# Performance work log

Hardware: AMD Instinct MI355X
Metric: run time of the kernel (lower is better)

Reference implementation:

```python
import jax, jax.numpy as jnp
import numpy as np


def _conv1x1(x, w, b):
    # x: (B,C,H,W), w: (O,C), b: (O,)
    return jnp.einsum('oc,bchw->bohw', w, x) + b[None, :, None, None]


def _avg_pool2(x):
    B, C, H, W = x.shape
    return x.reshape(B, C, H // 2, 2, W // 2, 2).mean(axis=(3, 5))


def setup_inputs() -> dict:
    key = jax.random.key(0)
    B, C, H, W = 8, 64, 64, 64
    ks = jax.random.split(key, 14)
    s = 1.0 / np.sqrt(C)

    def wb(k1, k2):
        return (jax.random.uniform(k1, (C, C), jnp.float32, -s, s),
                jax.random.uniform(k2, (C,), jnp.float32, -s, s))

    w_q, b_q = wb(ks[0], ks[1])
    w_K, b_K = wb(ks[2], ks[3])
    w_V, b_V = wb(ks[4], ks[5])
    w_Q, b_Q = wb(ks[6], ks[7])
    w_k, b_k = wb(ks[8], ks[9])
    w_v, b_v = wb(ks[10], ks[11])
    x = jax.random.normal(ks[12], (B, C, H, W), jnp.float32)
    gamma = jnp.ones((1,), jnp.float32)
    return dict(x=x, w_q=w_q, b_q=b_q, w_K=w_K, b_K=b_K, w_V=w_V, b_V=b_V,
                w_Q=w_Q, b_Q=b_Q, w_k=w_k, b_k=b_k, w_v=w_v, b_v=b_v,
                gamma=gamma)


def reference(x, w_q, b_q, w_K, b_K, w_V, b_V, w_Q, b_Q, w_k, b_k, w_v, b_v, gamma):
    B, C, H, W = x.shape
    N = H * W
    N4 = N // 4

    # Stage 1: pooled queries vs full key/value
    q = _conv1x1(x, w_q, b_q)                      # (B,C,H,W); torch views as (B,C,W,H) but H==W
    qp = _avg_pool2(q).reshape(B, C, N4).transpose(0, 2, 1)   # (B,N/4,C)
    Kf = _conv1x1(x, w_K, b_K).reshape(B, C, N)                # (B,C,N)
    Vf = _conv1x1(x, w_V, b_V).reshape(B, C, N)                # (B,C,N)
    attn = jax.nn.softmax(jnp.einsum('bnc,bcm->bnm', qp, Kf), axis=-1)  # (B,N/4,N)
    out = jnp.einsum('bcm,bnm->bcn', Vf, attn)                 # (B,C,N/4)
    out = out.reshape(B, C, H // 2, W // 2)

    # Stage 2: full queries vs pooled-derived key/value
    Qf = _conv1x1(x, w_Q, b_Q).reshape(B, C, N).transpose(0, 2, 1)  # (B,N,C)
    kp = _conv1x1(out, w_k, b_k).reshape(B, C, N4)                  # (B,C,N/4)
    vp = _conv1x1(out, w_v, b_v).reshape(B, C, N4)                  # (B,C,N/4)
    attn2 = jax.nn.softmax(jnp.einsum('bnc,bcm->bnm', Qf, kp), axis=-1)  # (B,N,N/4)
    out2 = jnp.einsum('bcm,bnm->bcn', vp, attn2).reshape(B, C, H, W)

    return gamma * out2 + x
```

## Files before the change

kernel.cpp:

```cpp
#include <hip/hip_runtime.h>
#include <math.h>


typedef __bf16 bf16;
typedef __attribute__((ext_vector_type(4))) __bf16 bf16x4;
typedef __attribute__((ext_vector_type(8))) __bf16 bf16x8;
typedef __attribute__((ext_vector_type(4))) float f32x4;

__device__ __forceinline__ void gl_lds16(const bf16* g, bf16* l) {
    __builtin_amdgcn_global_load_lds(
        (const __attribute__((address_space(1))) unsigned int*)g,
        (__attribute__((address_space(3))) unsigned int*)l,
        16, 0, 0);
}

__device__ __forceinline__ void proj_wave(
    const bf16* __restrict__ src, int TN,
    const float* __restrict__ W, const float* __restrict__ Bs,
    bf16* __restrict__ Y, int tr, int N, int b, int gn0, int lane)
{
    const int c16 = lane & 15, q4 = lane >> 4;
    bf16x8 wa[4][2];
    #pragma unroll
    for (int to = 0; to < 4; ++to)
        #pragma unroll
        for (int h = 0; h < 2; ++h) {
            const float* wp = W + (16 * to + c16) * 64 + q4 * 8 + 32 * h;
            float4 f0 = *(const float4*)wp;
            float4 f1 = *(const float4*)(wp + 4);
            bf16 tmp[8] = {(bf16)f0.x, (bf16)f0.y, (bf16)f0.z, (bf16)f0.w,
                           (bf16)f1.x, (bf16)f1.y, (bf16)f1.z, (bf16)f1.w};
            wa[to][h] = *(bf16x8*)tmp;
        }
    for (int tn = 0; tn < TN; ++tn) {
        bf16x8 xb0 = *(const bf16x8*)&src[(16 * tn + c16) * 72 + q4 * 8];
        bf16x8 xb1 = *(const bf16x8*)&src[(16 * tn + c16) * 72 + q4 * 8 + 32];
        #pragma unroll
        for (int to = 0; to < 4; ++to) {
            f32x4 acc = (f32x4){0.f, 0.f, 0.f, 0.f};
            acc = __builtin_amdgcn_mfma_f32_16x16x32_bf16(wa[to][0], xb0, acc, 0, 0, 0);
            acc = __builtin_amdgcn_mfma_f32_16x16x32_bf16(wa[to][1], xb1, acc, 0, 0, 0);
            if (tr) {
                float4 b4 = *(const float4*)(Bs + 16 * to + q4 * 4);
                bf16x4 yv;
                yv[0] = (bf16)(acc[0] + b4.x); yv[1] = (bf16)(acc[1] + b4.y);
                yv[2] = (bf16)(acc[2] + b4.z); yv[3] = (bf16)(acc[3] + b4.w);
                *(bf16x4*)(Y + ((size_t)b * N + gn0 + 16 * tn + c16) * 64 + 16 * to + q4 * 4) = yv;
            } else {
                float4 b4 = *(const float4*)(Bs + 16 * to + q4 * 4);
                float bias[4] = {b4.x, b4.y, b4.z, b4.w};
                #pragma unroll
                for (int r = 0; r < 4; ++r)
                    Y[((size_t)b * 64 + 16 * to + q4 * 4 + r) * N + gn0 + 16 * tn + c16] =
                        (bf16)(acc[r] + bias[r]);
            }
        }
    }
}

__global__ __launch_bounds__(256) void prep_kernel(
    const float* __restrict__ x,
    const float* __restrict__ w_K, const float* __restrict__ b_K, bf16* __restrict__ Kt,
    const float* __restrict__ w_Q, const float* __restrict__ b_Q, bf16* __restrict__ Qt,
    const float* __restrict__ w_V, const float* __restrict__ b_V, bf16* __restrict__ Vf,
    const float* __restrict__ w_q, const float* __restrict__ b_q, bf16* __restrict__ qpt)
{
    __shared__ float tile[128 * 65];
    __shared__ __align__(16) bf16 xbT[128 * 72];
    __shared__ __align__(16) bf16 xpb[32 * 72];
    const int t  = threadIdx.x;
    const int h2 = blockIdx.x;
    const int b  = blockIdx.y;
    const int n0 = h2 * 128;

    #pragma unroll
    for (int i = 0; i < 32; ++i) {
        int lin = i * 256 + t;
        int n = lin & 127, c = lin >> 7;
        tile[n * 65 + c] = x[((size_t)b * 64 + c) * 4096 + n0 + n];
    }
    __syncthreads();
    #pragma unroll
    for (int i = 0; i < 4; ++i) {
        int slot = i * 256 + t;
        int n = slot >> 3, c0 = (slot & 7) * 8;
        bf16 tmp[8];
        #pragma unroll
        for (int j = 0; j < 8; ++j) tmp[j] = (bf16)tile[n * 65 + c0 + j];
        *(bf16x8*)&xbT[n * 72 + c0] = *(bf16x8*)tmp;
    }
    {
        int wp = t & 31, c0 = (t >> 5) * 8;
        bf16 tmp[8];
        #pragma unroll
        for (int j = 0; j < 8; ++j) {
            float a = tile[(2 * wp) * 65 + c0 + j] + tile[(2 * wp + 1) * 65 + c0 + j]
                    + tile[(64 + 2 * wp) * 65 + c0 + j] + tile[(64 + 2 * wp + 1) * 65 + c0 + j];
            tmp[j] = (bf16)(0.25f * a);
        }
        *(bf16x8*)&xpb[wp * 72 + c0] = *(bf16x8*)tmp;
    }
    __syncthreads();

    const int lane = t & 63;
    const int w    = t >> 6;
    {
        const int mat  = w >> 1;
        const int half = w & 1;
        proj_wave(xbT + half * 64 * 72, 4,
                  mat == 0 ? w_K : w_Q, mat == 0 ? b_K : b_Q,
                  mat == 0 ? Kt : Qt, 1, 4096, b, n0 + half * 64, lane);
    }
    if (w < 2) {
        proj_wave(xbT + w * 64 * 72, 4, w_V, b_V, Vf, 0, 4096, b, n0 + w * 64, lane);
    } else if (w == 2) {
        proj_wave(xpb, 2, w_q, b_q, qpt, 1, 1024, b, h2 * 32, lane);
    }
}

template<int NSPLIT, int MODE, int U>
__global__ __launch_bounds__(256, 3) void flash_kernel(
    const bf16* __restrict__ Qt, const bf16* __restrict__ Kt,
    const bf16* __restrict__ Vn, int NQ, int L,
    bf16* __restrict__ Opart, float* __restrict__ Lbuf,
    float* __restrict__ out_f, const float* __restrict__ resid,
    const float* __restrict__ gamma_p)
{
    const int tid  = threadIdx.x;
    const int lane = tid & 63;
    const int w    = tid >> 6;
    const int c16  = lane & 15;
    const int q4   = lane >> 4;
    const int b    = blockIdx.y;
    const int n0   = blockIdx.x * (64 * U) + w * (16 * U);
    const int s    = (NSPLIT > 1) ? blockIdx.z : 0;
    const int SL   = L / NSPLIT;
    const int k0   = s * SL;
    const int ntiles = SL / 64;

    __shared__ __align__(16) bf16 Ks[2][64 * 64];
    __shared__ __align__(16) bf16 Vs[2][64 * 64];
    __shared__ __align__(16) bf16 Pw[4][16 * U * 72];

    const int rl8 = lane >> 3;
    const int cg  = ((lane & 7) - rl8) & 7;

    const bf16* Kb = Kt + (size_t)b * L * 64;
    const bf16* Vb = Vn + (size_t)b * 64 * L;

    bf16x8 bq[U][2];
    #pragma unroll
    for (int u = 0; u < U; ++u) {
        const bf16* qrow = Qt + ((size_t)b * NQ + n0 + 16 * u + c16) * 64 + q4 * 8;
        bq[u][0] = *(const bf16x8*)(qrow);
        bq[u][1] = *(const bf16x8*)(qrow + 32);
    }

    f32x4 O[U][4];
    #pragma unroll
    for (int u = 0; u < U; ++u)
        #pragma unroll
        for (int g = 0; g < 4; ++g) O[u][g] = (f32x4){0.f, 0.f, 0.f, 0.f};
    float l_acc[U];
    #pragma unroll
    for (int u = 0; u < U; ++u) l_acc[u] = 0.f;

    #pragma unroll
    for (int j = 0; j < 2; ++j) {
        const int row = 16 * w + 8 * j + rl8;
        gl_lds16(Kb + (size_t)(k0 + row) * 64 + cg * 8, &Ks[0][(16 * w + 8 * j) * 64]);
        gl_lds16(Vb + (size_t)row * L + k0 + cg * 8,    &Vs[0][(16 * w + 8 * j) * 64]);
    }
    __syncthreads();

    for (int it = 0; it < ntiles; ++it) {
        const int buf = it & 1;
        if (it + 1 < ntiles) {
            const int kn = k0 + (it + 1) * 64;
            #pragma unroll
            for (int j = 0; j < 2; ++j) {
                const int row = 16 * w + 8 * j + rl8;
                gl_lds16(Kb + (size_t)(kn + row) * 64 + cg * 8, &Ks[buf ^ 1][(16 * w + 8 * j) * 64]);
                gl_lds16(Vb + (size_t)row * L + kn + cg * 8,    &Vs[buf ^ 1][(16 * w + 8 * j) * 64]);
            }
        }

        f32x4 sv[U][4];
        #pragma unroll
        for (int t = 0; t < 4; ++t) {
            const bf16* krow = &Ks[buf][(16 * t + c16) * 64];
            bf16x8 ak0 = *(const bf16x8*)&krow[((q4 + c16) & 7) * 8];
            bf16x8 ak1 = *(const bf16x8*)&krow[((q4 + 4 + c16) & 7) * 8];
            #pragma unroll
            for (int u = 0; u < U; ++u) {
                f32x4 z = (f32x4){0.f, 0.f, 0.f, 0.f};
                z = __builtin_amdgcn_mfma_f32_16x16x32_bf16(ak0, bq[u][0], z, 0, 0, 0);
                sv[u][t] = __builtin_amdgcn_mfma_f32_16x16x32_bf16(ak1, bq[u][1], z, 0, 0, 0);
            }
        }

        #pragma unroll
        for (int u = 0; u < U; ++u) {
            #pragma unroll
            for (int t = 0; t < 4; ++t) {
                #pragma unroll
                for (int r = 0; r < 4; ++r) {
                    float p = __expf(sv[u][t][r]);
                    sv[u][t][r] = p;
                    l_acc[u] += p;
                }
                bf16x4 pv;
                pv[0] = (bf16)sv[u][t][0]; pv[1] = (bf16)sv[u][t][1];
                pv[2] = (bf16)sv[u][t][2]; pv[3] = (bf16)sv[u][t][3];
                *(bf16x4*)&Pw[w][(16 * u + c16) * 72 + 16 * t + 4 * q4] = pv;
            }
        }

        #pragma unroll
        for (int h = 0; h < 2; ++h) {
            bf16x8 pf[U];
            #pragma unroll
            for (int u = 0; u < U; ++u)
                pf[u] = *(const bf16x8*)&Pw[w][(16 * u + c16) * 72 + 32 * h + 8 * q4];
            #pragma unroll
            for (int g = 0; g < 4; ++g) {
                bf16x8 av = *(const bf16x8*)&Vs[buf][(16 * g + c16) * 64 + ((4 * h + q4 + c16) & 7) * 8];
                #pragma unroll
                for (int u = 0; u < U; ++u)
                    O[u][g] = __builtin_amdgcn_mfma_f32_16x16x32_bf16(av, pf[u], O[u][g], 0, 0, 0);
            }
        }
        __syncthreads();
    }

    float l_tot[U];
    #pragma unroll
    for (int u = 0; u < U; ++u) {
        float l = l_acc[u];
        l += __shfl_xor(l, 16);
        l += __shfl_xor(l, 32);
        l_tot[u] = l;
    }

    if (MODE == 2) {
        const float gm = gamma_p[0];
        #pragma unroll
        for (int u = 0; u < U; ++u) {
            float inv = gm / l_tot[u];
            const int n = n0 + 16 * u + c16;
            #pragma unroll
            for (int g = 0; g < 4; ++g) {
                #pragma unroll
                for (int r = 0; r < 4; ++r) {
                    size_t oidx = ((size_t)b * 64 + 16 * g + 4 * q4 + r) * NQ + n;
                    out_f[oidx] = O[u][g][r] * inv + resid[oidx];
                }
            }
        }
    } else {
        #pragma unroll
        for (int u = 0; u < U; ++u) {
            float inv = 1.0f / l_tot[u];
            bf16* dst = Opart + ((size_t)(b * NSPLIT + s) * NQ + n0 + 16 * u + c16) * 64 + q4 * 4;
            #pragma unroll
            for (int g = 0; g < 4; ++g) {
                bf16x4 yv;
                #pragma unroll
                for (int r = 0; r < 4; ++r) yv[r] = (bf16)(O[u][g][r] * inv);
                *(bf16x4*)(dst + 16 * g) = yv;
            }
        }
        if (lane < 16) {
            #pragma unroll
            for (int u = 0; u < U; ++u)
                Lbuf[(b * NSPLIT + s) * NQ + n0 + 16 * u + lane] = l_tot[u];
        }
    }
}

__global__ __launch_bounds__(256) void comb1kv_kernel(
    const bf16* __restrict__ Opart, const float* __restrict__ Lbuf,
    const float* __restrict__ w_k, const float* __restrict__ b_k, bf16* __restrict__ kpt,
    const float* __restrict__ w_v, const float* __restrict__ b_v, bf16* __restrict__ vp)
{
    __shared__ __align__(16) bf16 tile[32 * 72];
    __shared__ float wbuf[32 * 8];
    const int t  = threadIdx.x;
    const int m0 = blockIdx.x * 32;
    const int b  = blockIdx.y;

    if (t < 32) {
        int m = m0 + t;
        float ls[8], lt = 0.f;
        #pragma unroll
        for (int s = 0; s < 8; ++s) {
            ls[s] = Lbuf[(b * 8 + s) * 1024 + m];
            lt += ls[s];
        }
        float inv = 1.f / lt;
        #pragma unroll
        for (int s = 0; s < 8; ++s) wbuf[t * 8 + s] = ls[s] * inv;
    }
    __syncthreads();

    #pragma unroll
    for (int i = 0; i < 2; ++i) {
        int ml = i * 16 + (t >> 4);
        int c4 = (t & 15) * 4;
        const bf16* base = Opart + ((size_t)(b * 8) * 1024 + m0 + ml) * 64 + c4;
        float a0 = 0.f, a1 = 0.f, a2 = 0.f, a3 = 0.f;
        #pragma unroll
        for (int s = 0; s < 8; ++s) {
            bf16x4 v = *(const bf16x4*)(base + (size_t)s * 1024 * 64);
            float wg = wbuf[ml * 8 + s];
            a0 += (float)v[0] * wg; a1 += (float)v[1] * wg;
            a2 += (float)v[2] * wg; a3 += (float)v[3] * wg;
        }
        bf16x4 o; o[0] = (bf16)a0; o[1] = (bf16)a1; o[2] = (bf16)a2; o[3] = (bf16)a3;
        *(bf16x4*)&tile[ml * 72 + c4] = o;
    }
    __syncthreads();

    const int lane = t & 63;
    const int w    = t >> 6;
    const int c16 = lane & 15, q4 = lane >> 4;

    if (w < 2) {
        bf16x8 wb[4][2];
        #pragma unroll
        for (int to = 0; to < 4; ++to)
            #pragma unroll
            for (int h = 0; h < 2; ++h) {
                const float* wp = w_k + (16 * to + c16) * 64 + q4 * 8 + 32 * h;
                float4 f0 = *(const float4*)wp;
                float4 f1 = *(const float4*)(wp + 4);
                bf16 tmp[8] = {(bf16)f0.x, (bf16)f0.y, (bf16)f0.z, (bf16)f0.w,
                               (bf16)f1.x, (bf16)f1.y, (bf16)f1.z, (bf16)f1.w};
                wb[to][h] = *(bf16x8*)tmp;
            }
        const int tm = w;
        bf16x8 a0 = *(const bf16x8*)&tile[(16 * tm + c16) * 72 + q4 * 8];
        bf16x8 a1 = *(const bf16x8*)&tile[(16 * tm + c16) * 72 + q4 * 8 + 32];
        #pragma unroll
        for (int to = 0; to < 4; ++to) {
            f32x4 acc = (f32x4){0.f, 0.f, 0.f, 0.f};
            acc = __builtin_amdgcn_mfma_f32_16x16x32_bf16(a0, wb[to][0], acc, 0, 0, 0);
            acc = __builtin_amdgcn_mfma_f32_16x16x32_bf16(a1, wb[to][1], acc, 0, 0, 0);
            float bias = b_k[16 * to + c16];
            #pragma unroll
            for (int r = 0; r < 4; ++r)
                kpt[((size_t)b * 1024 + m0 + 16 * tm + 4 * q4 + r) * 64 + 16 * to + c16] =
                    (bf16)(acc[r] + bias);
        }
    } else {
        bf16x8 wa[4][2];
        #pragma unroll
        for (int ta = 0; ta < 4; ++ta)
            #pragma unroll
            for (int h = 0; h < 2; ++h) {
                const float* wp = w_v + (16 * ta + c16) * 64 + q4 * 8 + 32 * h;
                float4 f0 = *(const float4*)wp;
                float4 f1 = *(const float4*)(wp + 4);
                bf16 tmp[8] = {(bf16)f0.x, (bf16)f0.y, (bf16)f0.z, (bf16)f0.w,
                               (bf16)f1.x, (bf16)f1.y, (bf16)f1.z, (bf16)f1.w};
                wa[ta][h] = *(bf16x8*)tmp;
            }
        const int tm = w - 2;
        bf16x8 bb0 = *(const bf16x8*)&tile[(16 * tm + c16) * 72 + q4 * 8];
        bf16x8 bb1 = *(const bf16x8*)&tile[(16 * tm + c16) * 72 + q4 * 8 + 32];
        #pragma unroll
        for (int ta = 0; ta < 4; ++ta) {
            f32x4 acc = (f32x4){0.f, 0.f, 0.f, 0.f};
            acc = __builtin_amdgcn_mfma_f32_16x16x32_bf16(wa[ta][0], bb0, acc, 0, 0, 0);
            acc = __builtin_amdgcn_mfma_f32_16x16x32_bf16(wa[ta][1], bb1, acc, 0, 0, 0);
            float4 b4 = *(const float4*)(b_v + 16 * ta + 4 * q4);
            float bias[4] = {b4.x, b4.y, b4.z, b4.w};
            #pragma unroll
            for (int r = 0; r < 4; ++r)
                vp[((size_t)b * 64 + 16 * ta + 4 * q4 + r) * 1024 + m0 + 16 * tm + c16] =
                    (bf16)(acc[r] + bias[r]);
        }
    }
}

extern "C" void kernel_launch(void* const* d_in, const int* in_sizes, int n_in,
                              void* d_out, int out_size, void* d_ws, size_t ws_size,
                              hipStream_t stream) {
    const float* x    = (const float*)d_in[0];
    const float* w_q  = (const float*)d_in[1];
    const float* b_q  = (const float*)d_in[2];
    const float* w_K  = (const float*)d_in[3];
    const float* b_K  = (const float*)d_in[4];
    const float* w_V  = (const float*)d_in[5];
    const float* b_V  = (const float*)d_in[6];
    const float* w_Q  = (const float*)d_in[7];
    const float* b_Q  = (const float*)d_in[8];
    const float* w_k  = (const float*)d_in[9];
    const float* b_k  = (const float*)d_in[10];
    const float* w_v  = (const float*)d_in[11];
    const float* b_v  = (const float*)d_in[12];
    const float* gamma = (const float*)d_in[13];
    float* out = (float*)d_out;

    char* ws = (char*)d_ws;
    bf16*  Kt    = (bf16*)ws;   ws += (size_t)8 * 4096 * 64 * 2;
    bf16*  Qt    = (bf16*)ws;   ws += (size_t)8 * 4096 * 64 * 2;
    bf16*  Vf    = (bf16*)ws;   ws += (size_t)8 * 4096 * 64 * 2;
    bf16*  qpt   = (bf16*)ws;   ws += (size_t)8 * 1024 * 64 * 2;
    bf16*  kpt   = (bf16*)ws;   ws += (size_t)8 * 1024 * 64 * 2;
    bf16*  vp    = (bf16*)ws;   ws += (size_t)8 * 64 * 1024 * 2;
    bf16*  Opart = (bf16*)ws;   ws += (size_t)8 * 8 * 1024 * 64 * 2;
    float* Lb    = (float*)ws;  ws += (size_t)8 * 8 * 1024 * 4;

    prep_kernel<<<dim3(32, 8), 256, 0, stream>>>(
        x, w_K, b_K, Kt, w_Q, b_Q, Qt, w_V, b_V, Vf, w_q, b_q, qpt);

    flash_kernel<8, 1, 1><<<dim3(16, 8, 8), 256, 0, stream>>>(
        qpt, Kt, Vf, 1024, 4096, Opart, Lb, nullptr, nullptr, nullptr);

    comb1kv_kernel<<<dim3(32, 8), 256, 0, stream>>>(
        Opart, Lb, w_k, b_k, kpt, w_v, b_v, vp);

    flash_kernel<1, 2, 1><<<dim3(64, 8, 1), 256, 0, stream>>>(
        Qt, kpt, vp, 4096, 1024, nullptr, nullptr, out, x, gamma);
}
```

Measured before the change: 137.3 us.

## Split stage-2 attention over keys and add fp32 combine kernel

Stage-2 flash attention now splits the 1024 keys into two partitions. Each partition writes normalized fp32 partial outputs and row sums to workspace, and a new combine kernel merges them, transposes through LDS, applies gamma and adds the residual. Stage 1 also changes its template tile parameter and halves its grid's x dimension. The split is meant to raise parallelism for the under-occupied stage-2 launch, at the cost of an extra kernel launch and an extra fp32 round trip of the output through global memory.

```diff
diff --git a/kernel.cpp b/kernel.cpp
--- a/kernel.cpp
+++ b/kernel.cpp
@@ -261,13 +261,24 @@
         #pragma unroll
         for (int u = 0; u < U; ++u) {
             float inv = 1.0f / l_tot[u];
-            bf16* dst = Opart + ((size_t)(b * NSPLIT + s) * NQ + n0 + 16 * u + c16) * 64 + q4 * 4;
-            #pragma unroll
-            for (int g = 0; g < 4; ++g) {
-                bf16x4 yv;
-                #pragma unroll
-                for (int r = 0; r < 4; ++r) yv[r] = (bf16)(O[u][g][r] * inv);
-                *(bf16x4*)(dst + 16 * g) = yv;
+            if (MODE == 1) {
+                bf16* dst = Opart + ((size_t)(b * NSPLIT + s) * NQ + n0 + 16 * u + c16) * 64 + q4 * 4;
+                #pragma unroll
+                for (int g = 0; g < 4; ++g) {
+                    bf16x4 yv;
+                    #pragma unroll
+                    for (int r = 0; r < 4; ++r) yv[r] = (bf16)(O[u][g][r] * inv);
+                    *(bf16x4*)(dst + 16 * g) = yv;
+                }
+            } else {
+                float* dst = out_f + ((size_t)(b * NSPLIT + s) * NQ + n0 + 16 * u + c16) * 64 + q4 * 4;
+                #pragma unroll
+                for (int g = 0; g < 4; ++g) {
+                    float4 yv;
+                    yv.x = O[u][g][0] * inv; yv.y = O[u][g][1] * inv;
+                    yv.z = O[u][g][2] * inv; yv.w = O[u][g][3] * inv;
+                    *(float4*)(dst + 16 * g) = yv;
+                }
             }
         }
         if (lane < 16) {
@@ -380,6 +391,49 @@
                 vp[((size_t)b * 64 + 16 * ta + 4 * q4 + r) * 1024 + m0 + 16 * tm + c16] =
                     (bf16)(acc[r] + bias[r]);
         }
+    }
+}
+
+__global__ __launch_bounds__(256) void comb2_kernel(
+    const float* __restrict__ Of2, const float* __restrict__ Lb2,
+    const float* __restrict__ x, const float* __restrict__ gamma_p,
+    float* __restrict__ out)
+{
+    __shared__ float tile[64][65];
+    __shared__ float wt[64][2];
+    const int t  = threadIdx.x;
+    const int q0 = blockIdx.x * 64;
+    const int b  = blockIdx.y;
+
+    if (t < 64) {
+        float l0 = Lb2[((size_t)b * 2 + 0) * 4096 + q0 + t];
+        float l1 = Lb2[((size_t)b * 2 + 1) * 4096 + q0 + t];
+        float inv = 1.f / (l0 + l1);
+        wt[t][0] = l0 * inv; wt[t][1] = l1 * inv;
+    }
+    __syncthreads();
+
+    #pragma unroll
+    for (int i = 0; i < 4; ++i) {
+        int lin = i * 256 + t;
+        int q = lin >> 4, c4 = (lin & 15) * 4;
+        float w0 = wt[q][0], w1 = wt[q][1];
+        float4 v0 = *(const float4*)&Of2[(((size_t)b * 2 + 0) * 4096 + q0 + q) * 64 + c4];
+        float4 v1 = *(const float4*)&Of2[(((size_t)b * 2 + 1) * 4096 + q0 + q) * 64 + c4];
+        tile[q][c4 + 0] = w0 * v0.x + w1 * v1.x;
+        tile[q][c4 + 1] = w0 * v0.y + w1 * v1.y;
+        tile[q][c4 + 2] = w0 * v0.z + w1 * v1.z;
+        tile[q][c4 + 3] = w0 * v0.w + w1 * v1.w;
+    }
+    __syncthreads();
+
+    const float gm = gamma_p[0];
+    const int wv = t >> 6, ln = t & 63;
+    #pragma unroll
+    for (int cc = 0; cc < 16; ++cc) {
+        int c = wv * 16 + cc;
+        size_t o = ((size_t)b * 64 + c) * 4096 + q0 + ln;
+        out[o] = gm * tile[ln][c] + x[o];
     }
 }
 
@@ -411,16 +465,21 @@
     bf16*  vp    = (bf16*)ws;   ws += (size_t)8 * 64 * 1024 * 2;
     bf16*  Opart = (bf16*)ws;   ws += (size_t)8 * 8 * 1024 * 64 * 2;
     float* Lb    = (float*)ws;  ws += (size_t)8 * 8 * 1024 * 4;
+    float* Of2   = (float*)ws;  ws += (size_t)8 * 2 * 4096 * 64 * 4;
+    float* Lb2   = (float*)ws;  ws += (size_t)8 * 2 * 4096 * 4;
 
     prep_kernel<<<dim3(32, 8), 256, 0, stream>>>(
         x, w_K, b_K, Kt, w_Q, b_Q, Qt, w_V, b_V, Vf, w_q, b_q, qpt);
 
-    flash_kernel<8, 1, 1><<<dim3(16, 8, 8), 256, 0, stream>>>(
+    flash_kernel<8, 1, 2><<<dim3(8, 8, 8), 256, 0, stream>>>(
         qpt, Kt, Vf, 1024, 4096, Opart, Lb, nullptr, nullptr, nullptr);
 
     comb1kv_kernel<<<dim3(32, 8), 256, 0, stream>>>(
         Opart, Lb, w_k, b_k, kpt, w_v, b_v, vp);
 
-    flash_kernel<1, 2, 1><<<dim3(64, 8, 1), 256, 0, stream>>>(
-        Qt, kpt, vp, 4096, 1024, nullptr, nullptr, out, x, gamma);
-}
+    flash_kernel<2, 3, 2><<<dim3(32, 8, 2), 256, 0, stream>>>(
+        Qt, kpt, vp, 4096, 1024, nullptr, Lb2, Of2, nullptr, nullptr);
+
+    comb2_kernel<<<dim3(64, 8), 256, 0, stream>>>(
+        Of2, Lb2, x, gamma, out);
+}
```

New measurement: 142.8 us. 1.04x slower.

## Fold K/V/Q projections into pooled side via algebraic reassociation

Applied to the files above, without the earlier changes.

Stops materialising the full-resolution K, V and Q projections. Stage 1 now attends raw bf16 x against the query premultiplied by W_K^T, and applies W_V after the softmax-weighted sum of x. The K-bias term cancels in softmax, and the Q-bias enters stage 2 as a per-key additive bias. The flash kernel also gains U=2 query unrolling and, for stage 2, a 512-thread two-way key split with an LDS reduction. This removes three large projection GEMMs and their bf16 writes, in exchange for extra small projections in the combine kernel and a bias load in the inner loop.

```diff
diff --git a/kernel.cpp b/kernel.cpp
--- a/kernel.cpp
+++ b/kernel.cpp
@@ -14,45 +14,69 @@
         16, 0, 0);
 }
 
-__device__ __forceinline__ void proj_wave(
-    const bf16* __restrict__ src, int TN,
-    const float* __restrict__ W, const float* __restrict__ Bs,
-    bf16* __restrict__ Y, int tr, int N, int b, int gn0, int lane)
+struct WFrag { bf16x8 f[4][2]; };
+
+template<int WT>
+__device__ __forceinline__ WFrag load_wfrag(const float* __restrict__ W, int lane) {
+    const int c16 = lane & 15, q4 = lane >> 4;
+    WFrag wf;
+    #pragma unroll
+    for (int to = 0; to < 4; ++to)
+        #pragma unroll
+        for (int h = 0; h < 2; ++h) {
+            bf16 tmp[8];
+            if (WT == 0) {
+                const float* wp = W + (16 * to + c16) * 64 + q4 * 8 + 32 * h;
+                float4 f0 = *(const float4*)wp;
+                float4 f1 = *(const float4*)(wp + 4);
+                tmp[0] = (bf16)f0.x; tmp[1] = (bf16)f0.y;
+                tmp[2] = (bf16)f0.z; tmp[3] = (bf16)f0.w;
+                tmp[4] = (bf16)f1.x; tmp[5] = (bf16)f1.y;
+                tmp[6] = (bf16)f1.z; tmp[7] = (bf16)f1.w;
+            } else {
+                #pragma unroll
+                for (int j = 0; j < 8; ++j)
+                    tmp[j] = (bf16)W[(q4 * 8 + 32 * h + j) * 64 + 16 * to + c16];
+            }
+            wf.f[to][h] = *(bf16x8*)tmp;
+        }
+    return wf;
+}
+
+template<int OUT>
+__device__ __forceinline__ void proj_run(
+    const bf16* __restrict__ src, int TN, const WFrag& wf, const float* __restrict__ Bs,
+    bf16* __restrict__ Y, int N, int b, int gn0, bf16* __restrict__ Yl, int lane)
 {
     const int c16 = lane & 15, q4 = lane >> 4;
-    bf16x8 wa[4][2];
-    #pragma unroll
-    for (int to = 0; to < 4; ++to)
-        #pragma unroll
-        for (int h = 0; h < 2; ++h) {
-            const float* wp = W + (16 * to + c16) * 64 + q4 * 8 + 32 * h;
-            float4 f0 = *(const float4*)wp;
-            float4 f1 = *(const float4*)(wp + 4);
-            bf16 tmp[8] = {(bf16)f0.x, (bf16)f0.y, (bf16)f0.z, (bf16)f0.w,
-                           (bf16)f1.x, (bf16)f1.y, (bf16)f1.z, (bf16)f1.w};
-            wa[to][h] = *(bf16x8*)tmp;
-        }
     for (int tn = 0; tn < TN; ++tn) {
         bf16x8 xb0 = *(const bf16x8*)&src[(16 * tn + c16) * 72 + q4 * 8];
         bf16x8 xb1 = *(const bf16x8*)&src[(16 * tn + c16) * 72 + q4 * 8 + 32];
         #pragma unroll
         for (int to = 0; to < 4; ++to) {
             f32x4 acc = (f32x4){0.f, 0.f, 0.f, 0.f};
-            acc = __builtin_amdgcn_mfma_f32_16x16x32_bf16(wa[to][0], xb0, acc, 0, 0, 0);
-            acc = __builtin_amdgcn_mfma_f32_16x16x32_bf16(wa[to][1], xb1, acc, 0, 0, 0);
-            if (tr) {
+            acc = __builtin_amdgcn_mfma_f32_16x16x32_bf16(wf.f[to][0], xb0, acc, 0, 0, 0);
+            acc = __builtin_amdgcn_mfma_f32_16x16x32_bf16(wf.f[to][1], xb1, acc, 0, 0, 0);
+            float bias[4] = {0.f, 0.f, 0.f, 0.f};
+            if (Bs) {
                 float4 b4 = *(const float4*)(Bs + 16 * to + q4 * 4);
+                bias[0] = b4.x; bias[1] = b4.y; bias[2] = b4.z; bias[3] = b4.w;
+            }
+            if (OUT == 0) {
                 bf16x4 yv;
-                yv[0] = (bf16)(acc[0] + b4.x); yv[1] = (bf16)(acc[1] + b4.y);
-                yv[2] = (bf16)(acc[2] + b4.z); yv[3] = (bf16)(acc[3] + b4.w);
-                *(bf16x4*)(Y + ((size_t)b * N + gn0 + 16 * tn + c16) * 64 + 16 * to + q4 * 4) = yv;
+                #pragma unroll
+                for (int r = 0; r < 4; ++r) yv[r] = (bf16)(acc[r] + bias[r]);
+                *(bf16x4*)(Y + ((size_t)b * N + gn0 + 16 * tn + c16) * 64 + 16 * to + 4 * q4) = yv;
+            } else if (OUT == 1) {
+                #pragma unroll
+                for (int r = 0; r < 4; ++r)
+                    Y[((size_t)b * 64 + 16 * to + 4 * q4 + r) * N + gn0 + 16 * tn + c16] =
+                        (bf16)(acc[r] + bias[r]);
             } else {
-                float4 b4 = *(const float4*)(Bs + 16 * to + q4 * 4);
-                float bias[4] = {b4.x, b4.y, b4.z, b4.w};
-                #pragma unroll
-                for (int r = 0; r < 4; ++r)
-                    Y[((size_t)b * 64 + 16 * to + q4 * 4 + r) * N + gn0 + 16 * tn + c16] =
-                        (bf16)(acc[r] + bias[r]);
+                bf16x4 yv;
+                #pragma unroll
+                for (int r = 0; r < 4; ++r) yv[r] = (bf16)(acc[r] + bias[r]);
+                *(bf16x4*)&Yl[(16 * tn + c16) * 72 + 16 * to + 4 * q4] = yv;
             }
         }
     }
@@ -60,14 +84,13 @@
 
 __global__ __launch_bounds__(256) void prep_kernel(
     const float* __restrict__ x,
-    const float* __restrict__ w_K, const float* __restrict__ b_K, bf16* __restrict__ Kt,
-    const float* __restrict__ w_Q, const float* __restrict__ b_Q, bf16* __restrict__ Qt,
-    const float* __restrict__ w_V, const float* __restrict__ b_V, bf16* __restrict__ Vf,
-    const float* __restrict__ w_q, const float* __restrict__ b_q, bf16* __restrict__ qpt)
+    const float* __restrict__ w_q, const float* __restrict__ b_q,
+    const float* __restrict__ w_K,
+    bf16* __restrict__ xt, bf16* __restrict__ xn, bf16* __restrict__ qkt)
 {
     __shared__ float tile[128 * 65];
-    __shared__ __align__(16) bf16 xbT[128 * 72];
     __shared__ __align__(16) bf16 xpb[32 * 72];
+    __shared__ __align__(16) bf16 qtile[32 * 72];
     const int t  = threadIdx.x;
     const int h2 = blockIdx.x;
     const int b  = blockIdx.y;
@@ -80,6 +103,19 @@
         tile[n * 65 + c] = x[((size_t)b * 64 + c) * 4096 + n0 + n];
     }
     __syncthreads();
+    {
+        int wp = t & 31, c0 = (t >> 5) * 8;
+        bf16 tmp[8];
+        #pragma unroll
+        for (int j = 0; j < 8; ++j) {
+            float a = tile[(2 * wp) * 65 + c0 + j] + tile[(2 * wp + 1) * 65 + c0 + j]
+                    + tile[(64 + 2 * wp) * 65 + c0 + j] + tile[(64 + 2 * wp + 1) * 65 + c0 + j];
+            tmp[j] = (bf16)(0.25f * a);
+        }
+        *(bf16x8*)&xpb[wp * 72 + c0] = *(bf16x8*)tmp;
+    }
+    __syncthreads();
+
     #pragma unroll
     for (int i = 0; i < 4; ++i) {
         int slot = i * 256 + t;
@@ -87,60 +123,52 @@
         bf16 tmp[8];
         #pragma unroll
         for (int j = 0; j < 8; ++j) tmp[j] = (bf16)tile[n * 65 + c0 + j];
-        *(bf16x8*)&xbT[n * 72 + c0] = *(bf16x8*)tmp;
-    }
-    {
-        int wp = t & 31, c0 = (t >> 5) * 8;
+        *(bf16x8*)&xt[((size_t)b * 4096 + n0 + n) * 64 + c0] = *(bf16x8*)tmp;
+    }
+    #pragma unroll
+    for (int i = 0; i < 4; ++i) {
+        int slot = i * 256 + t;
+        int c = slot >> 4, n8 = slot & 15;
         bf16 tmp[8];
         #pragma unroll
-        for (int j = 0; j < 8; ++j) {
-            float a = tile[(2 * wp) * 65 + c0 + j] + tile[(2 * wp + 1) * 65 + c0 + j]
-                    + tile[(64 + 2 * wp) * 65 + c0 + j] + tile[(64 + 2 * wp + 1) * 65 + c0 + j];
-            tmp[j] = (bf16)(0.25f * a);
-        }
-        *(bf16x8*)&xpb[wp * 72 + c0] = *(bf16x8*)tmp;
-    }
-    __syncthreads();
-
-    const int lane = t & 63;
-    const int w    = t >> 6;
-    {
-        const int mat  = w >> 1;
-        const int half = w & 1;
-        proj_wave(xbT + half * 64 * 72, 4,
-                  mat == 0 ? w_K : w_Q, mat == 0 ? b_K : b_Q,
-                  mat == 0 ? Kt : Qt, 1, 4096, b, n0 + half * 64, lane);
-    }
-    if (w < 2) {
-        proj_wave(xbT + w * 64 * 72, 4, w_V, b_V, Vf, 0, 4096, b, n0 + w * 64, lane);
-    } else if (w == 2) {
-        proj_wave(xpb, 2, w_q, b_q, qpt, 1, 1024, b, h2 * 32, lane);
-    }
-}
-
-template<int NSPLIT, int MODE, int U>
-__global__ __launch_bounds__(256, 3) void flash_kernel(
+        for (int j = 0; j < 8; ++j) tmp[j] = (bf16)tile[(n8 * 8 + j) * 65 + c];
+        *(bf16x8*)&xn[((size_t)b * 64 + c) * 4096 + n0 + n8 * 8] = *(bf16x8*)tmp;
+    }
+    if ((t >> 6) == 3) {
+        const int lane = t & 63;
+        WFrag wfq  = load_wfrag<0>(w_q, lane);
+        WFrag wfKT = load_wfrag<1>(w_K, lane);
+        proj_run<2>(xpb, 2, wfq, b_q, nullptr, 0, 0, 0, qtile, lane);
+        asm volatile("s_waitcnt lgkmcnt(0)" ::: "memory");
+        proj_run<0>(qtile, 2, wfKT, nullptr, qkt, 1024, b, h2 * 32, nullptr, lane);
+    }
+}
+
+template<int NSPLIT, int MODE, int U, int KS, bool BIAS>
+__global__ __launch_bounds__(256 * KS, KS == 1 ? 3 : 2) void flash_kernel(
     const bf16* __restrict__ Qt, const bf16* __restrict__ Kt,
     const bf16* __restrict__ Vn, int NQ, int L,
     bf16* __restrict__ Opart, float* __restrict__ Lbuf,
     float* __restrict__ out_f, const float* __restrict__ resid,
-    const float* __restrict__ gamma_p)
+    const float* __restrict__ gamma_p, const float* __restrict__ Gb)
 {
     const int tid  = threadIdx.x;
     const int lane = tid & 63;
     const int w    = tid >> 6;
+    const int wl   = w & 3;
+    const int g    = w >> 2;
     const int c16  = lane & 15;
     const int q4   = lane >> 4;
     const int b    = blockIdx.y;
-    const int n0   = blockIdx.x * (64 * U) + w * (16 * U);
+    const int n0   = blockIdx.x * (64 * U) + wl * (16 * U);
     const int s    = (NSPLIT > 1) ? blockIdx.z : 0;
-    const int SL   = L / NSPLIT;
-    const int k0   = s * SL;
+    const int SL   = L / (NSPLIT * KS);
+    const int k0   = (s * KS + g) * SL;
     const int ntiles = SL / 64;
 
-    __shared__ __align__(16) bf16 Ks[2][64 * 64];
-    __shared__ __align__(16) bf16 Vs[2][64 * 64];
-    __shared__ __align__(16) bf16 Pw[4][16 * U * 72];
+    __shared__ __align__(16) bf16 Ks[KS][2][64 * 64];
+    __shared__ __align__(16) bf16 Vs[KS][2][64 * 64];
+    __shared__ __align__(16) bf16 Pw[4 * KS][16 * U * 72];
 
     const int rl8 = lane >> 3;
     const int cg  = ((lane & 7) - rl8) & 7;
@@ -160,16 +188,16 @@
     #pragma unroll
     for (int u = 0; u < U; ++u)
         #pragma unroll
-        for (int g = 0; g < 4; ++g) O[u][g] = (f32x4){0.f, 0.f, 0.f, 0.f};
+        for (int gi = 0; gi < 4; ++gi) O[u][gi] = (f32x4){0.f, 0.f, 0.f, 0.f};
     float l_acc[U];
     #pragma unroll
     for (int u = 0; u < U; ++u) l_acc[u] = 0.f;
 
     #pragma unroll
     for (int j = 0; j < 2; ++j) {
-        const int row = 16 * w + 8 * j + rl8;
-        gl_lds16(Kb + (size_t)(k0 + row) * 64 + cg * 8, &Ks[0][(16 * w + 8 * j) * 64]);
-        gl_lds16(Vb + (size_t)row * L + k0 + cg * 8,    &Vs[0][(16 * w + 8 * j) * 64]);
+        const int row = 16 * wl + 8 * j + rl8;
+        gl_lds16(Kb + (size_t)(k0 + row) * 64 + cg * 8, &Ks[g][0][(16 * wl + 8 * j) * 64]);
+        gl_lds16(Vb + (size_t)row * L + k0 + cg * 8,    &Vs[g][0][(16 * wl + 8 * j) * 64]);
     }
     __syncthreads();
 
@@ -179,16 +207,16 @@
             const int kn = k0 + (it + 1) * 64;
             #pragma unroll
             for (int j = 0; j < 2; ++j) {
-                const int row = 16 * w + 8 * j + rl8;
-                gl_lds16(Kb + (size_t)(kn + row) * 64 + cg * 8, &Ks[buf ^ 1][(16 * w + 8 * j) * 64]);
-                gl_lds16(Vb + (size_t)row * L + kn + cg * 8,    &Vs[buf ^ 1][(16 * w + 8 * j) * 64]);
+                const int row = 16 * wl + 8 * j + rl8;
+                gl_lds16(Kb + (size_t)(kn + row) * 64 + cg * 8, &Ks[g][buf ^ 1][(16 * wl + 8 * j) * 64]);
+                gl_lds16(Vb + (size_t)row * L + kn + cg * 8,    &Vs[g][buf ^ 1][(16 * wl + 8 * j) * 64]);
             }
         }
 
         f32x4 sv[U][4];
         #pragma unroll
         for (int t = 0; t < 4; ++t) {
-            const bf16* krow = &Ks[buf][(16 * t + c16) * 64];
+            const bf16* krow = &Ks[g][buf][(16 * t + c16) * 64];
             bf16x8 ak0 = *(const bf16x8*)&krow[((q4 + c16) & 7) * 8];
             bf16x8 ak1 = *(const bf16x8*)&krow[((q4 + 4 + c16) & 7) * 8];
             #pragma unroll
@@ -199,13 +227,22 @@
             }
         }
 
+        float4 gb[4];
+        if (BIAS) {
+            #pragma unroll
+            for (int t = 0; t < 4; ++t)
+                gb[t] = *(const float4*)&Gb[(size_t)b * 1024 + k0 + it * 64 + 16 * t + 4 * q4];
+        }
+
         #pragma unroll
         for (int u = 0; u < U; ++u) {
             #pragma unroll
             for (int t = 0; t < 4; ++t) {
                 #pragma unroll
                 for (int r = 0; r < 4; ++r) {
-                    float p = __expf(sv[u][t][r]);
+                    float sval = sv[u][t][r];
+                    if (BIAS) sval += ((const float*)&gb[t])[r];
+                    float p = __expf(sval);
                     sv[u][t][r] = p;
                     l_acc[u] += p;
                 }
@@ -223,11 +260,11 @@
             for (int u = 0; u < U; ++u)
                 pf[u] = *(const bf16x8*)&Pw[w][(16 * u + c16) * 72 + 32 * h + 8 * q4];
             #pragma unroll
-            for (int g = 0; g < 4; ++g) {
-                bf16x8 av = *(const bf16x8*)&Vs[buf][(16 * g + c16) * 64 + ((4 * h + q4 + c16) & 7) * 8];
+            for (int gi = 0; gi < 4; ++gi) {
+                bf16x8 av = *(const bf16x8*)&Vs[g][buf][(16 * gi + c16) * 64 + ((4 * h + q4 + c16) & 7) * 8];
                 #pragma unroll
                 for (int u = 0; u < U; ++u)
-                    O[u][g] = __builtin_amdgcn_mfma_f32_16x16x32_bf16(av, pf[u], O[u][g], 0, 0, 0);
+                    O[u][gi] = __builtin_amdgcn_mfma_f32_16x16x32_bf16(av, pf[u], O[u][gi], 0, 0, 0);
             }
         }
         __syncthreads();
@@ -242,6 +279,33 @@
         l_tot[u] = l;
     }
 
+    if (KS == 2) {
+        float* sc = (float*)&Pw[0][0];
+        const int base = (wl * 64 + lane) * 34;
+        if (g == 1) {
+            #pragma unroll
+            for (int u = 0; u < U; ++u) {
+                #pragma unroll
+                for (int gi = 0; gi < 4; ++gi)
+                    #pragma unroll
+                    for (int r = 0; r < 4; ++r)
+                        sc[base + u * 16 + gi * 4 + r] = O[u][gi][r];
+                sc[base + 32 + u] = l_tot[u];
+            }
+        }
+        __syncthreads();
+        if (g == 1) return;
+        #pragma unroll
+        for (int u = 0; u < U; ++u) {
+            #pragma unroll
+            for (int gi = 0; gi < 4; ++gi)
+                #pragma unroll
+                for (int r = 0; r < 4; ++r)
+                    O[u][gi][r] += sc[base + u * 16 + gi * 4 + r];
+            l_tot[u] += sc[base + 32 + u];
+        }
+    }
+
     if (MODE == 2) {
         const float gm = gamma_p[0];
         #pragma unroll
@@ -249,11 +313,11 @@
             float inv = gm / l_tot[u];
             const int n = n0 + 16 * u + c16;
             #pragma unroll
-            for (int g = 0; g < 4; ++g) {
+            for (int gi = 0; gi < 4; ++gi) {
                 #pragma unroll
                 for (int r = 0; r < 4; ++r) {
-                    size_t oidx = ((size_t)b * 64 + 16 * g + 4 * q4 + r) * NQ + n;
-                    out_f[oidx] = O[u][g][r] * inv + resid[oidx];
+                    size_t oidx = ((size_t)b * 64 + 16 * gi + 4 * q4 + r) * NQ + n;
+                    out_f[oidx] = O[u][gi][r] * inv + resid[oidx];
                 }
             }
         }
@@ -263,11 +327,11 @@
             float inv = 1.0f / l_tot[u];
             bf16* dst = Opart + ((size_t)(b * NSPLIT + s) * NQ + n0 + 16 * u + c16) * 64 + q4 * 4;
             #pragma unroll
-            for (int g = 0; g < 4; ++g) {
+            for (int gi = 0; gi < 4; ++gi) {
                 bf16x4 yv;
                 #pragma unroll
-                for (int r = 0; r < 4; ++r) yv[r] = (bf16)(O[u][g][r] * inv);
-                *(bf16x4*)(dst + 16 * g) = yv;
+                for (int r = 0; r < 4; ++r) yv[r] = (bf16)(O[u][gi][r] * inv);
+                *(bf16x4*)(dst + 16 * gi) = yv;
             }
         }
         if (lane < 16) {
@@ -280,14 +344,27 @@
 
 __global__ __launch_bounds__(256) void comb1kv_kernel(
     const bf16* __restrict__ Opart, const float* __restrict__ Lbuf,
-    const float* __restrict__ w_k, const float* __restrict__ b_k, bf16* __restrict__ kpt,
-    const float* __restrict__ w_v, const float* __restrict__ b_v, bf16* __restrict__ vp)
+    const float* __restrict__ w_V, const float* __restrict__ b_V,
+    const float* __restrict__ w_k, const float* __restrict__ b_k,
+    const float* __restrict__ w_v, const float* __restrict__ b_v,
+    const float* __restrict__ w_Q, const float* __restrict__ b_Q,
+    bf16* __restrict__ qk2t, bf16* __restrict__ vp, float* __restrict__ Gb)
 {
     __shared__ __align__(16) bf16 tile[32 * 72];
+    __shared__ __align__(16) bf16 otile[32 * 72];
+    __shared__ __align__(16) bf16 kpl[32 * 72];
     __shared__ float wbuf[32 * 8];
     const int t  = threadIdx.x;
     const int m0 = blockIdx.x * 32;
     const int b  = blockIdx.y;
+    const int w  = t >> 6;
+    const int lane = t & 63;
+
+    WFrag wf;
+    if      (w == 0) wf = load_wfrag<0>(w_V, lane);
+    else if (w == 1) wf = load_wfrag<0>(w_k, lane);
+    else if (w == 2) wf = load_wfrag<0>(w_v, lane);
+    else             wf = load_wfrag<1>(w_Q, lane);
 
     if (t < 32) {
         int m = m0 + t;
@@ -321,65 +398,17 @@
     }
     __syncthreads();
 
-    const int lane = t & 63;
-    const int w    = t >> 6;
-    const int c16 = lane & 15, q4 = lane >> 4;
-
-    if (w < 2) {
-        bf16x8 wb[4][2];
-        #pragma unroll
-        for (int to = 0; to < 4; ++to)
-            #pragma unroll
-            for (int h = 0; h < 2; ++h) {
-                const float* wp = w_k + (16 * to + c16) * 64 + q4 * 8 + 32 * h;
-                float4 f0 = *(const float4*)wp;
-                float4 f1 = *(const float4*)(wp + 4);
-                bf16 tmp[8] = {(bf16)f0.x, (bf16)f0.y, (bf16)f0.z, (bf16)f0.w,
-                               (bf16)f1.x, (bf16)f1.y, (bf16)f1.z, (bf16)f1.w};
-                wb[to][h] = *(bf16x8*)tmp;
-            }
-        const int tm = w;
-        bf16x8 a0 = *(const bf16x8*)&tile[(16 * tm + c16) * 72 + q4 * 8];
-        bf16x8 a1 = *(const bf16x8*)&tile[(16 * tm + c16) * 72 + q4 * 8 + 32];
-        #pragma unroll
-        for (int to = 0; to < 4; ++to) {
-            f32x4 acc = (f32x4){0.f, 0.f, 0.f, 0.f};
-            acc = __builtin_amdgcn_mfma_f32_16x16x32_bf16(a0, wb[to][0], acc, 0, 0, 0);
-            acc = __builtin_amdgcn_mfma_f32_16x16x32_bf16(a1, wb[to][1], acc, 0, 0, 0);
-            float bias = b_k[16 * to + c16];
-            #pragma unroll
-            for (int r = 0; r < 4; ++r)
-                kpt[((size_t)b * 1024 + m0 + 16 * tm + 4 * q4 + r) * 64 + 16 * to + c16] =
-                    (bf16)(acc[r] + bias);
-        }
-    } else {
-        bf16x8 wa[4][2];
-        #pragma unroll
-        for (int ta = 0; ta < 4; ++ta)
-            #pragma unroll
-            for (int h = 0; h < 2; ++h) {
-                const float* wp = w_v + (16 * ta + c16) * 64 + q4 * 8 + 32 * h;
-                float4 f0 = *(const float4*)wp;
-                float4 f1 = *(const float4*)(wp + 4);
-                bf16 tmp[8] = {(bf16)f0.x, (bf16)f0.y, (bf16)f0.z, (bf16)f0.w,
-                               (bf16)f1.x, (bf16)f1.y, (bf16)f1.z, (bf16)f1.w};
-                wa[ta][h] = *(bf16x8*)tmp;
-            }
-        const int tm = w - 2;
-        bf16x8 bb0 = *(const bf16x8*)&tile[(16 * tm + c16) * 72 + q4 * 8];
-        bf16x8 bb1 = *(const bf16x8*)&tile[(16 * tm + c16) * 72 + q4 * 8 + 32];
-        #pragma unroll
-        for (int ta = 0; ta < 4; ++ta) {
-            f32x4 acc = (f32x4){0.f, 0.f, 0.f, 0.f};
-            acc = __builtin_amdgcn_mfma_f32_16x16x32_bf16(wa[ta][0], bb0, acc, 0, 0, 0);
-            acc = __builtin_amdgcn_mfma_f32_16x16x32_bf16(wa[ta][1], bb1, acc, 0, 0, 0);
-            float4 b4 = *(const float4*)(b_v + 16 * ta + 4 * q4);
-            float bias[4] = {b4.x, b4.y, b4.z, b4.w};
-            #pragma unroll
-            for (int r = 0; r < 4; ++r)
-                vp[((size_t)b * 64 + 16 * ta + 4 * q4 + r) * 1024 + m0 + 16 * tm + c16] =
-                    (bf16)(acc[r] + bias[r]);
-        }
+    if (w == 0) proj_run<2>(tile, 2, wf, b_V, nullptr, 0, 0, 0, otile, lane);
+    __syncthreads();
+    if (w == 1) proj_run<2>(otile, 2, wf, b_k, nullptr, 0, 0, 0, kpl, lane);
+    if (w == 2) proj_run<1>(otile, 2, wf, b_v, vp, 1024, b, m0, nullptr, lane);
+    __syncthreads();
+    if (w == 3) proj_run<0>(kpl, 2, wf, nullptr, qk2t, 1024, b, m0, nullptr, lane);
+    if (w == 0 && lane < 32) {
+        float acc = 0.f;
+        #pragma unroll
+        for (int c = 0; c < 64; ++c) acc += b_Q[c] * (float)kpl[lane * 72 + c];
+        Gb[(size_t)b * 1024 + m0 + lane] = acc;
     }
 }
 
@@ -390,7 +419,7 @@
     const float* w_q  = (const float*)d_in[1];
     const float* b_q  = (const float*)d_in[2];
     const float* w_K  = (const float*)d_in[3];
-    const float* b_K  = (const float*)d_in[4];
+    const float* b_K  = (const float*)d_in[4];   (void)b_K;
     const float* w_V  = (const float*)d_in[5];
     const float* b_V  = (const float*)d_in[6];
     const float* w_Q  = (const float*)d_in[7];
@@ -403,24 +432,23 @@
     float* out = (float*)d_out;
 
     char* ws = (char*)d_ws;
-    bf16*  Kt    = (bf16*)ws;   ws += (size_t)8 * 4096 * 64 * 2;
-    bf16*  Qt    = (bf16*)ws;   ws += (size_t)8 * 4096 * 64 * 2;
-    bf16*  Vf    = (bf16*)ws;   ws += (size_t)8 * 4096 * 64 * 2;
-    bf16*  qpt   = (bf16*)ws;   ws += (size_t)8 * 1024 * 64 * 2;
-    bf16*  kpt   = (bf16*)ws;   ws += (size_t)8 * 1024 * 64 * 2;
+    bf16*  xt    = (bf16*)ws;   ws += (size_t)8 * 4096 * 64 * 2;
+    bf16*  xn    = (bf16*)ws;   ws += (size_t)8 * 4096 * 64 * 2;
+    bf16*  qkt   = (bf16*)ws;   ws += (size_t)8 * 1024 * 64 * 2;
+    bf16*  qk2t  = (bf16*)ws;   ws += (size_t)8 * 1024 * 64 * 2;
     bf16*  vp    = (bf16*)ws;   ws += (size_t)8 * 64 * 1024 * 2;
     bf16*  Opart = (bf16*)ws;   ws += (size_t)8 * 8 * 1024 * 64 * 2;
     float* Lb    = (float*)ws;  ws += (size_t)8 * 8 * 1024 * 4;
-
-    prep_kernel<<<dim3(32, 8), 256, 0, stream>>>(
-        x, w_K, b_K, Kt, w_Q, b_Q, Qt, w_V, b_V, Vf, w_q, b_q, qpt);
-
-    flash_kernel<8, 1, 1><<<dim3(16, 8, 8), 256, 0, stream>>>(
-        qpt, Kt, Vf, 1024, 4096, Opart, Lb, nullptr, nullptr, nullptr);
+    float* Gb    = (float*)ws;  ws += (size_t)8 * 1024 * 4;
+
+    prep_kernel<<<dim3(32, 8), 256, 0, stream>>>(x, w_q, b_q, w_K, xt, xn, qkt);
+
+    flash_kernel<8, 1, 2, 1, false><<<dim3(8, 8, 8), 256, 0, stream>>>(
+        qkt, xt, xn, 1024, 4096, Opart, Lb, nullptr, nullptr, nullptr, nullptr);
 
     comb1kv_kernel<<<dim3(32, 8), 256, 0, stream>>>(
-        Opart, Lb, w_k, b_k, kpt, w_v, b_v, vp);
-
-    flash_kernel<1, 2, 1><<<dim3(64, 8, 1), 256, 0, stream>>>(
-        Qt, kpt, vp, 4096, 1024, nullptr, nullptr, out, x, gamma);
-}
+        Opart, Lb, w_V, b_V, w_k, b_k, w_v, b_v, w_Q, b_Q, qk2t, vp, Gb);
+
+    flash_kernel<1, 2, 2, 2, true><<<dim3(32, 8, 1), 512, 0, stream>>>(
+        xt, qk2t, vp, 4096, 1024, nullptr, nullptr, out, x, gamma, Gb);
+}
```

Result: no change. 135.0 us (-1.7%).
